# Performance work log

Measured on AMD Instinct MI355X. Metric: run time of the kernel, lower is better.

The kernel has to match this reference:

```python
import jax, jax.numpy as jnp
import numpy as np

K = 16            # neighbors
QUERY_CHUNK = 256 # SE is applied per chunk of this many query points (matches torch loop)
EPS = 1e-5        # BatchNorm eps (eval mode, running stats)


def bn(x, g, b, m, v):
    # eval-mode batchnorm over last axis (channel-last layout here)
    return (x - m) * (g / jnp.sqrt(v + EPS)) + b


def setup_inputs() -> dict:
    key = jax.random.key(0)
    ks = jax.random.split(key, 16)
    B, Cin, N = 4, 128, 4096
    H, Cout = 128, 256
    se_h = Cout // 4
    r = lambda k, s, sc=1.0: jax.random.normal(k, s, jnp.float32) * sc
    return dict(
        x=r(ks[0], (B, Cin, N)),
        W_edge=r(ks[1], (H, 2 * Cin), 0.05),          # edge_mlp conv2d 1x1
        bn1_g=jnp.ones((H,), jnp.float32), bn1_b=jnp.zeros((H,), jnp.float32),
        bn1_m=r(ks[2], (H,), 0.1), bn1_v=jax.random.uniform(ks[3], (H,), jnp.float32) + 0.5,
        w_att=r(ks[4], (H,), 0.1),                     # att_conv (1,H,1,1)
        W_fuse=r(ks[5], (Cout, H), 0.05),              # fuse conv1d
        bn2_g=jnp.ones((Cout,), jnp.float32), bn2_b=jnp.zeros((Cout,), jnp.float32),
        bn2_m=r(ks[6], (Cout,), 0.1), bn2_v=jax.random.uniform(ks[7], (Cout,), jnp.float32) + 0.5,
        fc1_w=r(ks[8], (se_h, Cout), 0.05), fc1_b=jnp.zeros((se_h,), jnp.float32),
        fc2_w=r(ks[9], (Cout, se_h), 0.05), fc2_b=jnp.zeros((Cout,), jnp.float32),
        W_res=r(ks[10], (Cout, Cin), 0.05),            # res_conv conv1d (in!=out)
        bn3_g=jnp.ones((Cout,), jnp.float32), bn3_b=jnp.zeros((Cout,), jnp.float32),
        bn3_m=r(ks[11], (Cout,), 0.1), bn3_v=jax.random.uniform(ks[12], (Cout,), jnp.float32) + 0.5,
    )


def reference(x, W_edge, bn1_g, bn1_b, bn1_m, bn1_v, w_att,
              W_fuse, bn2_g, bn2_b, bn2_m, bn2_v,
              fc1_w, fc1_b, fc2_w, fc2_b,
              W_res, bn3_g, bn3_b, bn3_m, bn3_v):
    B, Cin, N = x.shape
    x_t = jnp.swapaxes(x, 1, 2)  # (B,N,Cin)

    # KNN on features (dynamic=False -> knn on x.transpose); squared euclidean
    # has the same ordering as torch.cdist(p=2).
    sq = jnp.sum(x_t * x_t, axis=-1)                               # (B,N)
    d2 = sq[:, :, None] + sq[:, None, :] - 2.0 * jnp.einsum('bnc,bmc->bnm', x_t, x_t)
    _, idx = jax.lax.top_k(-d2, K)                                  # (B,N,K) smallest dists

    neigh = jax.vmap(lambda p, i: p[i])(x_t, idx)                   # (B,N,K,Cin)
    center = jnp.broadcast_to(x_t[:, :, None, :], neigh.shape)      # (B,N,K,Cin)
    edge = jnp.concatenate([neigh - center, center], axis=-1)       # (B,N,K,2Cin)

    # edge_mlp: 1x1 conv + BN + ReLU
    h = jax.nn.relu(bn(jnp.einsum('bnkc,hc->bnkh', edge, W_edge),
                       bn1_g, bn1_b, bn1_m, bn1_v))                 # (B,N,K,H)

    # attention over neighbors
    att = jax.nn.softmax(jnp.einsum('bnkh,h->bnk', h, w_att), axis=-1)
    agg = jnp.einsum('bnkh,bnk->bnh', h, att)                       # (B,N,H)

    # fuse conv1d + BN + ReLU
    out = jax.nn.relu(bn(jnp.einsum('bnh,oh->bno', agg, W_fuse),
                         bn2_g, bn2_b, bn2_m, bn2_v))               # (B,N,Cout)

    # SE channel attention, applied per query chunk (matches torch loop semantics)
    Cout = out.shape[-1]
    nc = N // QUERY_CHUNK
    oc = out.reshape(B, nc, QUERY_CHUNK, Cout)
    s = oc.mean(axis=2)                                             # (B,nc,Cout)
    s = jax.nn.relu(jnp.einsum('bmc,hc->bmh', s, fc1_w) + fc1_b)
    s = jax.nn.sigmoid(jnp.einsum('bmh,ch->bmc', s, fc2_w) + fc2_b)
    out = (oc * s[:, :, None, :]).reshape(B, N, Cout)

    # residual projection (in_channels != out_channels)
    res = bn(jnp.einsum('bnc,oc->bno', x_t, W_res), bn3_g, bn3_b, bn3_m, bn3_v)
    out = out + res
    return jnp.swapaxes(out, 1, 2)                                  # (B,Cout,N)
```

## Files before the change

### kernel.cpp

```cpp
#include <hip/hip_runtime.h>
#include <cstddef>

typedef __bf16 bf16;
typedef __bf16 bf16x8 __attribute__((ext_vector_type(8)));
typedef float  f32x4  __attribute__((ext_vector_type(4)));
typedef unsigned short u16;
typedef unsigned long long u64;

#define MFMA16x16(a, b, c) __builtin_amdgcn_mfma_f32_16x16x32_bf16((a), (b), (c), 0, 0, 0)

namespace {
constexpr int BB   = 4;
constexpr int CIN  = 128;
constexpr int NPT  = 4096;
constexpr int KNBR = 16;
constexpr int HED  = 128;
constexpr int COUT = 256;
}

__device__ __forceinline__ double mk_keyd(float d, unsigned mlo ) {
  const u64 k = ((u64)__float_as_uint(d) << 32) | mlo;
  return __longlong_as_double((long long)k);
}
__device__ __forceinline__ int key_idx(double kd) {
  return (int)((__double_as_longlong(kd) >> 20) & 0xFFF);
}

__device__ __forceinline__ void sort16d(double* k) {
  #pragma unroll
  for (int sz = 2; sz <= 16; sz <<= 1) {
    #pragma unroll
    for (int st = sz >> 1; st > 0; st >>= 1) {
      #pragma unroll
      for (int i = 0; i < 16; ++i) {
        const int j = i ^ st;
        if (j > i) {
          const bool up = ((i & sz) == 0);
          const double a = k[i], c = k[j];
          const double lo = fmin(a, c), hi = fmax(a, c);
          k[i] = up ? lo : hi;
          k[j] = up ? hi : lo;
        }
      }
    }
  }
}

__device__ __forceinline__ void merge16d(double* R, const double* B) {
  double t[16];
  #pragma unroll
  for (int i = 0; i < 16; ++i) t[i] = fmin(R[i], B[15 - i]);
  #pragma unroll
  for (int st = 8; st > 0; st >>= 1) {
    #pragma unroll
    for (int i = 0; i < 16; ++i) {
      const int j = i ^ st;
      if (j > i) {
        const double a = t[i], c = t[j];
        t[i] = fmin(a, c);
        t[j] = fmax(a, c);
      }
    }
  }
  #pragma unroll
  for (int i = 0; i < 16; ++i) R[i] = t[i];
}

__device__ __forceinline__ void shfl_merge16d(double* R, int mask) {
  double B[16];
  #pragma unroll
  for (int i = 0; i < 16; ++i) B[i] = __shfl_xor(R[i], mask, 64);
  merge16d(R, B);
}

__global__ __launch_bounds__(256) void k_wconv(const float* __restrict__ We,
                                               const float* __restrict__ Wf,
                                               const float* __restrict__ Wr,
                                               bf16* __restrict__ Web,
                                               bf16* __restrict__ Wfb,
                                               bf16* __restrict__ Wrb) {
  const int i = blockIdx.x * 256 + threadIdx.x;
  const int a = i >> 15;
  const int j = i & 32767;
  const float* src = (a == 0) ? We : (a == 1) ? Wf : Wr;
  bf16*        dst = (a == 0) ? Web : (a == 1) ? Wfb : Wrb;
  dst[j] = (bf16)src[j];
}

__global__ __launch_bounds__(256) void k_prep(const float* __restrict__ x,
                                              bf16* __restrict__ xh,
                                              bf16* __restrict__ xl,
                                              float* __restrict__ sq) {
  __shared__ __attribute__((aligned(16))) bf16 th[64][136];
  __shared__ __attribute__((aligned(16))) bf16 tl[64][136];
  __shared__ float sqp[4][64];
  const int tid = threadIdx.x;
  const int b   = blockIdx.x >> 6;
  const int n0  = (blockIdx.x & 63) << 6;
  const int nl  = tid & 63;
  const int cg  = tid >> 6;
  const float* xb = x + (size_t)b * CIN * NPT;
  float acc = 0.f;
  #pragma unroll
  for (int rep = 0; rep < 32; ++rep) {
    const int c = rep * 4 + cg;
    const float v = xb[(size_t)c * NPT + n0 + nl];
    const bf16 h = (bf16)v;
    const bf16 l = (bf16)(v - (float)h);
    acc += v * v;
    th[nl][c] = h;
    tl[nl][c] = l;
  }
  sqp[cg][nl] = acc;
  __syncthreads();
  bf16* xho = xh + ((size_t)b * NPT + n0) * CIN;
  bf16* xlo = xl + ((size_t)b * NPT + n0) * CIN;
  #pragma unroll
  for (int rep = 0; rep < 32; ++rep) {
    const int e = rep * 256 + tid;
    const int r = e >> 7;
    const int c = e & 127;
    xho[(size_t)r * CIN + c] = th[r][c];
    xlo[(size_t)r * CIN + c] = tl[r][c];
  }
  if (tid < 64) {
    sq[b * NPT + n0 + tid] = sqp[0][tid] + sqp[1][tid] + sqp[2][tid] + sqp[3][tid];
  }
}

__global__ __launch_bounds__(256, 2) void k_knn(const bf16* __restrict__ xh,
                                                const bf16* __restrict__ xl,
                                                const float* __restrict__ sq,
                                                int* __restrict__ knn_idx) {
  __shared__ double Lk[32][66];
  const int tid  = threadIdx.x;
  const int w    = tid >> 6;
  const int lane = tid & 63;
  const int col  = lane & 15;
  const int quad = lane >> 4;
  const int b    = blockIdx.x >> 7;
  const int q0   = (blockIdx.x & 127) << 5;
  const bf16*  xhb = xh + (size_t)b * NPT * CIN;
  const bf16*  xlb = xl + (size_t)b * NPT * CIN;
  const float* sqb = sq + b * NPT;

  bf16x8 qh[2][4], ql[2][4];
  float sqn[2];
  #pragma unroll
  for (int t = 0; t < 2; ++t) {
    const bf16* qrh = xhb + (size_t)(q0 + t * 16 + col) * CIN + quad * 8;
    const bf16* qrl = xlb + (size_t)(q0 + t * 16 + col) * CIN + quad * 8;
    #pragma unroll
    for (int ks = 0; ks < 4; ++ks) {
      qh[t][ks] = *(const bf16x8*)(qrh + ks * 32);
      ql[t][ks] = *(const bf16x8*)(qrl + ks * 32);
    }
    sqn[t] = sqb[q0 + t * 16 + col];
  }

  const double INF = __builtin_inf();
  double R0[16], R1[16];
  #pragma unroll
  for (int i = 0; i < 16; ++i) { R0[i] = INF; R1[i] = INF; }

  const int cbase = w << 10;
  for (int mt = 0; mt < 16; ++mt) {
    const int m0 = cbase + (mt << 6);
    double k0[16], k1[16];
    #pragma unroll
    for (int cb = 0; cb < 4; ++cb) {
      const bf16* crh = xhb + (size_t)(m0 + cb * 16 + col) * CIN + quad * 8;
      const bf16* crl = xlb + (size_t)(m0 + cb * 16 + col) * CIN + quad * 8;
      f32x4 a0 = {0.f, 0.f, 0.f, 0.f};
      f32x4 a1 = {0.f, 0.f, 0.f, 0.f};
      #pragma unroll
      for (int ks = 0; ks < 4; ++ks) {
        const bf16x8 ch_ = *(const bf16x8*)(crh + ks * 32);
        const bf16x8 cl_ = *(const bf16x8*)(crl + ks * 32);
        a0 = MFMA16x16(cl_, qh[0][ks], a0);
        a0 = MFMA16x16(ch_, ql[0][ks], a0);
        a0 = MFMA16x16(ch_, qh[0][ks], a0);
        a1 = MFMA16x16(cl_, qh[1][ks], a1);
        a1 = MFMA16x16(ch_, ql[1][ks], a1);
        a1 = MFMA16x16(ch_, qh[1][ks], a1);
      }
      const f32x4 sqm = *(const f32x4*)(sqb + m0 + cb * 16 + quad * 4);
      const unsigned mlo0 = (unsigned)(m0 + cb * 16 + quad * 4) << 20;
      #pragma unroll
      for (int r = 0; r < 4; ++r) {
        k0[cb * 4 + r] = mk_keyd((sqn[0] + sqm[r]) - 2.0f * a0[r], mlo0 + ((unsigned)r << 20));
        k1[cb * 4 + r] = mk_keyd((sqn[1] + sqm[r]) - 2.0f * a1[r], mlo0 + ((unsigned)r << 20));
      }
    }
    sort16d(k0); merge16d(R0, k0);
    sort16d(k1); merge16d(R1, k1);
  }

  shfl_merge16d(R0, 16);
  shfl_merge16d(R0, 32);
  shfl_merge16d(R1, 16);
  shfl_merge16d(R1, 32);

  if (quad == 0) {
    #pragma unroll
    for (int i = 0; i < 16; ++i) {
      Lk[col][w * 16 + i]        = R0[i];
      Lk[16 | col][w * 16 + i]   = R1[i];
    }
  }
  __syncthreads();

  if (tid < 64) {
    const int q = tid >> 1;
    const int j = tid & 1;
    double A[16], Bv[16];
    #pragma unroll
    for (int i = 0; i < 16; ++i) {
      A[i]  = Lk[q][(2 * j) * 16 + i];
      Bv[i] = Lk[q][(2 * j + 1) * 16 + i];
    }
    merge16d(A, Bv);
    #pragma unroll
    for (int i = 0; i < 16; ++i) Lk[q][j * 16 + i] = A[i];
  }
  __syncthreads();
  if (tid < 32) {
    double A[16], Bv[16];
    #pragma unroll
    for (int i = 0; i < 16; ++i) {
      A[i]  = Lk[tid][i];
      Bv[i] = Lk[tid][16 + i];
    }
    merge16d(A, Bv);
    int* op = knn_idx + (size_t)(b * NPT + q0 + tid) * KNBR;
    #pragma unroll
    for (int i = 0; i < 16; ++i) op[i] = key_idx(A[i]);
  }
}

__global__ __launch_bounds__(256) void k_edge(const bf16* __restrict__ xh,
                                              const bf16* __restrict__ xl,
                                              const int* __restrict__ knn_idx,
                                              const bf16* __restrict__ We,
                                              const float* __restrict__ g1, const float* __restrict__ b1,
                                              const float* __restrict__ m1, const float* __restrict__ v1,
                                              const float* __restrict__ watt,
                                              bf16* __restrict__ agg) {
  __shared__ __attribute__((aligned(16))) bf16 Ew[4][16][264];
  __shared__ float s1[HED], t1[HED], wat[HED];
  const int tid  = threadIdx.x;
  const int w    = tid >> 6;
  const int lane = tid & 63;
  const int col  = lane & 15;
  const int quad = lane >> 4;
  if (tid < HED) {
    const float ss = g1[tid] / sqrtf(v1[tid] + 1e-5f);
    s1[tid] = ss;
    t1[tid] = b1[tid] - m1[tid] * ss;
    wat[tid] = watt[tid];
  }
  __syncthreads();
  const int p = blockIdx.x * 4 + w;
  const int b = p >> 12;
  const int n = p & 4095;
  const bf16* xhb = xh + (size_t)b * NPT * CIN;
  const bf16* xlb = xl + (size_t)b * NPT * CIN;
  const int my = knn_idx[(size_t)p * KNBR + col];
  const int m  = __shfl(my, lane >> 2);
  const int sub = lane & 3;
  const int kn  = lane >> 2;
  const bf16* nh = xhb + (size_t)m * CIN + sub * 32;
  const bf16* nl_ = xlb + (size_t)m * CIN + sub * 32;
  const bf16* ch = xhb + (size_t)n * CIN + sub * 32;
  const bf16* cl = xlb + (size_t)n * CIN + sub * 32;
  #pragma unroll
  for (int j = 0; j < 4; ++j) {
    const bf16x8 nhv = *(const bf16x8*)(nh + j * 8);
    const bf16x8 nlv = *(const bf16x8*)(nl_ + j * 8);
    const bf16x8 chv = *(const bf16x8*)(ch + j * 8);
    const bf16x8 clv = *(const bf16x8*)(cl + j * 8);
    bf16x8 dv, cv;
    #pragma unroll
    for (int e = 0; e < 8; ++e) {
      const float nf = (float)nhv[e] + (float)nlv[e];
      const float cf = (float)chv[e] + (float)clv[e];
      dv[e] = (bf16)(nf - cf);
      cv[e] = (bf16)cf;
    }
    *(bf16x8*)&Ew[w][kn][sub * 32 + j * 8]       = dv;
    *(bf16x8*)&Ew[w][kn][128 + sub * 32 + j * 8] = cv;
  }
  const f32x4 zero4 = {0.f, 0.f, 0.f, 0.f};
  f32x4 acc[8];
  #pragma unroll
  for (int hb = 0; hb < 8; ++hb) acc[hb] = zero4;
  #pragma unroll
  for (int ks = 0; ks < 8; ++ks) {
    const bf16x8 af = *(const bf16x8*)&Ew[w][col][ks * 32 + quad * 8];
    #pragma unroll
    for (int hb = 0; hb < 8; ++hb) {
      const bf16x8 bfv = *(const bf16x8*)(We + (size_t)(hb * 16 + col) * 256 + ks * 32 + quad * 8);
      acc[hb] = MFMA16x16(af, bfv, acc[hb]);
    }
  }
  float h[8][4];
  float lg[4] = {0.f, 0.f, 0.f, 0.f};
  #pragma unroll
  for (int hb = 0; hb < 8; ++hb) {
    const int hc = hb * 16 + col;
    const float ss = s1[hc], tt = t1[hc], ww = wat[hc];
    #pragma unroll
    for (int r = 0; r < 4; ++r) {
      const float hv = fmaxf(acc[hb][r] * ss + tt, 0.f);
      h[hb][r] = hv;
      lg[r] += hv * ww;
    }
  }
  #pragma unroll
  for (int r = 0; r < 4; ++r) {
    float vv = lg[r];
    vv += __shfl_xor(vv, 1);
    vv += __shfl_xor(vv, 2);
    vv += __shfl_xor(vv, 4);
    vv += __shfl_xor(vv, 8);
    lg[r] = vv;
  }
  float mx = fmaxf(fmaxf(lg[0], lg[1]), fmaxf(lg[2], lg[3]));
  mx = fmaxf(mx, __shfl_xor(mx, 16));
  mx = fmaxf(mx, __shfl_xor(mx, 32));
  float ex[4];
  float sm = 0.f;
  #pragma unroll
  for (int r = 0; r < 4; ++r) { ex[r] = expf(lg[r] - mx); sm += ex[r]; }
  sm += __shfl_xor(sm, 16);
  sm += __shfl_xor(sm, 32);
  const float inv = 1.0f / sm;
  float ag[8];
  #pragma unroll
  for (int hb = 0; hb < 8; ++hb) {
    float a = h[hb][0] * ex[0] + h[hb][1] * ex[1] + h[hb][2] * ex[2] + h[hb][3] * ex[3];
    a += __shfl_xor(a, 16);
    a += __shfl_xor(a, 32);
    ag[hb] = a * inv;
  }
  if (quad == 0) {
    bf16* ao = agg + (size_t)p * HED;
    #pragma unroll
    for (int hb = 0; hb < 8; ++hb) ao[hb * 16 + col] = (bf16)ag[hb];
  }
}

__global__ __launch_bounds__(256) void k_fuse(const bf16* __restrict__ agg,
                                              const bf16* __restrict__ Wf,
                                              const float* __restrict__ g2, const float* __restrict__ b2,
                                              const float* __restrict__ m2, const float* __restrict__ v2,
                                              bf16* __restrict__ outp) {
  const int tid  = threadIdx.x;
  const int w    = tid >> 6;
  const int lane = tid & 63;
  const int col  = lane & 15;
  const int quad = lane >> 4;
  const int pb   = blockIdx.x >> 2;
  const int obq  = blockIdx.x & 3;
  const int p0   = (pb * 4 + w) * 16;
  bf16x8 afr[4];
  const bf16* arow = agg + (size_t)(p0 + col) * HED + quad * 8;
  #pragma unroll
  for (int ks = 0; ks < 4; ++ks) afr[ks] = *(const bf16x8*)(arow + ks * 32);
  #pragma unroll
  for (int i = 0; i < 4; ++i) {
    const int ob = obq * 4 + i;
    f32x4 acc = {0.f, 0.f, 0.f, 0.f};
    const bf16* brow = Wf + (size_t)(ob * 16 + col) * HED + quad * 8;
    #pragma unroll
    for (int ks = 0; ks < 4; ++ks)
      acc = MFMA16x16(afr[ks], *(const bf16x8*)(brow + ks * 32), acc);
    const int o = ob * 16 + col;
    const float ss = g2[o] / sqrtf(v2[o] + 1e-5f);
    const float tt = b2[o] - m2[o] * ss;
    #pragma unroll
    for (int r = 0; r < 4; ++r) {
      outp[(size_t)(p0 + quad * 4 + r) * COUT + o] = (bf16)fmaxf(acc[r] * ss + tt, 0.f);
    }
  }
}

__global__ __launch_bounds__(256) void k_se1(const bf16* __restrict__ outp,
                                             float* __restrict__ part) {
  const int blk = blockIdx.x;
  const int tid = threadIdx.x;
  const bf16* base = outp + ((size_t)(blk >> 2) * 256 + (size_t)(blk & 3) * 64) * COUT;
  float s = 0.f;
  for (int p2 = 0; p2 < 64; ++p2) s += (float)base[(size_t)p2 * COUT + tid];
  part[(size_t)blk * COUT + tid] = s;
}

__global__ __launch_bounds__(256) void k_se2(const float* __restrict__ part,
                                             const float* __restrict__ f1w, const float* __restrict__ f1b,
                                             const float* __restrict__ f2w, const float* __restrict__ f2b,
                                             float* __restrict__ sse) {
  __shared__ float mean_s[COUT];
  __shared__ float h1[64];
  const int bc  = blockIdx.x;
  const int tid = threadIdx.x;
  const float* pb = part + (size_t)bc * 4 * COUT;
  mean_s[tid] = (pb[tid] + pb[COUT + tid] + pb[2 * COUT + tid] + pb[3 * COUT + tid]) * (1.0f / 256.0f);
  __syncthreads();
  if (tid < 64) {
    float a = f1b[tid];
    for (int c = 0; c < COUT; ++c) a += f1w[tid * COUT + c] * mean_s[c];
    h1[tid] = fmaxf(a, 0.f);
  }
  __syncthreads();
  float a = f2b[tid];
  #pragma unroll
  for (int j = 0; j < 64; ++j) a += f2w[tid * 64 + j] * h1[j];
  sse[(size_t)bc * COUT + tid] = 1.0f / (1.0f + expf(-a));
}

__global__ __launch_bounds__(256) void k_final(const bf16* __restrict__ xh,
                                               const bf16* __restrict__ Wr,
                                               const float* __restrict__ g3, const float* __restrict__ b3,
                                               const float* __restrict__ m3, const float* __restrict__ v3,
                                               const bf16* __restrict__ outp,
                                               const float* __restrict__ sse,
                                               float* __restrict__ out) {
  const int tid  = threadIdx.x;
  const int w    = tid >> 6;
  const int lane = tid & 63;
  const int col  = lane & 15;
  const int quad = lane >> 4;
  const int pb   = blockIdx.x >> 2;
  const int obq  = blockIdx.x & 3;
  const int p0   = (pb * 4 + w) * 16;
  const int b    = p0 >> 12;
  const int n0l  = p0 & 4095;
  bf16x8 afr[4];
  const bf16* arow = xh + (size_t)(p0 + col) * CIN + quad * 8;
  #pragma unroll
  for (int ks = 0; ks < 4; ++ks) afr[ks] = *(const bf16x8*)(arow + ks * 32);
  const float* scb = sse + (size_t)(b * 16 + (n0l >> 8)) * COUT;
  #pragma unroll
  for (int i = 0; i < 4; ++i) {
    const int ob = obq * 4 + i;
    f32x4 acc = {0.f, 0.f, 0.f, 0.f};
    const bf16* brow = Wr + (size_t)(ob * 16 + col) * CIN + quad * 8;
    #pragma unroll
    for (int ks = 0; ks < 4; ++ks)
      acc = MFMA16x16(afr[ks], *(const bf16x8*)(brow + ks * 32), acc);
    const int o = ob * 16 + col;
    const float ss = g3[o] / sqrtf(v3[o] + 1e-5f);
    const float tt = b3[o] - m3[o] * ss;
    const float sc = scb[o];
    f32x4 pk;
    #pragma unroll
    for (int r = 0; r < 4; ++r) {
      const float res = acc[r] * ss + tt;
      pk[r] = (float)outp[(size_t)(p0 + quad * 4 + r) * COUT + o] * sc + res;
    }
    float* op = out + (size_t)(b * COUT + o) * NPT + n0l + quad * 4;
    *(f32x4*)op = pk;
  }
}

extern "C" void kernel_launch(void* const* d_in, const int* in_sizes, int n_in,
                              void* d_out, int out_size, void* d_ws, size_t ws_size,
                              hipStream_t stream) {
  (void)in_sizes; (void)n_in; (void)out_size; (void)ws_size;
  const float* x    = (const float*)d_in[0];
  const float* We   = (const float*)d_in[1];
  const float* g1   = (const float*)d_in[2];
  const float* b1   = (const float*)d_in[3];
  const float* m1   = (const float*)d_in[4];
  const float* v1   = (const float*)d_in[5];
  const float* watt = (const float*)d_in[6];
  const float* Wf   = (const float*)d_in[7];
  const float* g2   = (const float*)d_in[8];
  const float* b2   = (const float*)d_in[9];
  const float* m2   = (const float*)d_in[10];
  const float* v2   = (const float*)d_in[11];
  const float* f1w  = (const float*)d_in[12];
  const float* f1b  = (const float*)d_in[13];
  const float* f2w  = (const float*)d_in[14];
  const float* f2b  = (const float*)d_in[15];
  const float* Wr   = (const float*)d_in[16];
  const float* g3   = (const float*)d_in[17];
  const float* b3   = (const float*)d_in[18];
  const float* m3   = (const float*)d_in[19];
  const float* v3   = (const float*)d_in[20];

  char* ws = (char*)d_ws;
  size_t off = 0;
  bf16*  xth  = (bf16*)(ws + off);  off += (size_t)BB * NPT * CIN * 2;
  bf16*  xtl  = (bf16*)(ws + off);  off += (size_t)BB * NPT * CIN * 2;
  float* sq   = (float*)(ws + off); off += (size_t)BB * NPT * 4;
  int*   idxp = (int*)(ws + off);   off += (size_t)BB * NPT * KNBR * 4;
  bf16*  aggp = (bf16*)(ws + off);  off += (size_t)BB * NPT * HED * 2;
  bf16*  outp = (bf16*)(ws + off);  off += (size_t)BB * NPT * COUT * 2;
  float* ssep = (float*)(ws + off); off += (size_t)BB * 16 * COUT * 4;
  float* partp= (float*)(ws + off); off += (size_t)256 * COUT * 4;
  bf16*  Web  = (bf16*)(ws + off);  off += (size_t)HED * 2 * CIN * 2;
  bf16*  Wfb  = (bf16*)(ws + off);  off += (size_t)COUT * HED * 2;
  bf16*  Wrb  = (bf16*)(ws + off);  off += (size_t)COUT * CIN * 2;

  float* out = (float*)d_out;

  k_wconv<<<384, 256, 0, stream>>>(We, Wf, Wr, Web, Wfb, Wrb);
  k_prep<<<256, 256, 0, stream>>>(x, xth, xtl, sq);
  k_knn<<<512, 256, 0, stream>>>(xth, xtl, sq, idxp);
  k_edge<<<4096, 256, 0, stream>>>(xth, xtl, idxp, Web, g1, b1, m1, v1, watt, aggp);
  k_fuse<<<1024, 256, 0, stream>>>(aggp, Wfb, g2, b2, m2, v2, outp);
  k_se1<<<256, 256, 0, stream>>>(outp, partp);
  k_se2<<<64, 256, 0, stream>>>(partp, f1w, f1b, f2w, f2b, ssep);
  k_final<<<1024, 256, 0, stream>>>(xth, Wrb, g3, b3, m3, v3, outp, ssep, out);
}
```

Baseline: 421.8 us.

## Merge weight conversion into prep, fold SE sums into fuse, batch edge points

Folds the weight bf16 conversion and zeroing of the SE partial buffer into the prep kernel as extra blocks. The SE channel sums are now accumulated by the fuse kernel with shuffles plus atomics, so the separate k_se1 pass over the output is gone. The edge kernel loops over four points per wave with a quarter of the blocks, which amortises the BN/attention table setup. The aim is fewer launches and one less read of the output; the cost is atomic contention and a reduction order that is no longer deterministic.

```diff
diff --git a/kernel.cpp b/kernel.cpp
--- a/kernel.cpp
+++ b/kernel.cpp
@@ -73,30 +73,37 @@
   merge16d(R, B);
 }
 
-__global__ __launch_bounds__(256) void k_wconv(const float* __restrict__ We,
+__global__ __launch_bounds__(256) void k_prepw(const float* __restrict__ x,
+                                               bf16* __restrict__ xh,
+                                               bf16* __restrict__ xl,
+                                               float* __restrict__ sq,
+                                               const float* __restrict__ We,
                                                const float* __restrict__ Wf,
                                                const float* __restrict__ Wr,
                                                bf16* __restrict__ Web,
                                                bf16* __restrict__ Wfb,
-                                               bf16* __restrict__ Wrb) {
-  const int i = blockIdx.x * 256 + threadIdx.x;
-  const int a = i >> 15;
-  const int j = i & 32767;
-  const float* src = (a == 0) ? We : (a == 1) ? Wf : Wr;
-  bf16*        dst = (a == 0) ? Web : (a == 1) ? Wfb : Wrb;
-  dst[j] = (bf16)src[j];
-}
-
-__global__ __launch_bounds__(256) void k_prep(const float* __restrict__ x,
-                                              bf16* __restrict__ xh,
-                                              bf16* __restrict__ xl,
-                                              float* __restrict__ sq) {
+                                               bf16* __restrict__ Wrb,
+                                               float* __restrict__ partp) {
   __shared__ __attribute__((aligned(16))) bf16 th[64][136];
   __shared__ __attribute__((aligned(16))) bf16 tl[64][136];
   __shared__ float sqp[4][64];
+  const int blk = blockIdx.x;
   const int tid = threadIdx.x;
-  const int b   = blockIdx.x >> 6;
-  const int n0  = (blockIdx.x & 63) << 6;
+  if (blk >= 256) {
+    if (blk < 640) {
+      const int i = (blk - 256) * 256 + tid;
+      const int a = i >> 15;
+      const int j = i & 32767;
+      const float* src = (a == 0) ? We : (a == 1) ? Wf : Wr;
+      bf16*        dst = (a == 0) ? Web : (a == 1) ? Wfb : Wrb;
+      dst[j] = (bf16)src[j];
+    } else {
+      for (int i = tid; i < 64 * COUT; i += 256) partp[i] = 0.f;
+    }
+    return;
+  }
+  const int b   = blk >> 6;
+  const int n0  = (blk & 63) << 6;
   const int nl  = tid & 63;
   const int cg  = tid >> 6;
   const float* xb = x + (size_t)b * CIN * NPT;
@@ -260,93 +267,96 @@
     wat[tid] = watt[tid];
   }
   __syncthreads();
-  const int p = blockIdx.x * 4 + w;
-  const int b = p >> 12;
-  const int n = p & 4095;
-  const bf16* xhb = xh + (size_t)b * NPT * CIN;
-  const bf16* xlb = xl + (size_t)b * NPT * CIN;
-  const int my = knn_idx[(size_t)p * KNBR + col];
-  const int m  = __shfl(my, lane >> 2);
-  const int sub = lane & 3;
-  const int kn  = lane >> 2;
-  const bf16* nh = xhb + (size_t)m * CIN + sub * 32;
-  const bf16* nl_ = xlb + (size_t)m * CIN + sub * 32;
-  const bf16* ch = xhb + (size_t)n * CIN + sub * 32;
-  const bf16* cl = xlb + (size_t)n * CIN + sub * 32;
-  #pragma unroll
-  for (int j = 0; j < 4; ++j) {
-    const bf16x8 nhv = *(const bf16x8*)(nh + j * 8);
-    const bf16x8 nlv = *(const bf16x8*)(nl_ + j * 8);
-    const bf16x8 chv = *(const bf16x8*)(ch + j * 8);
-    const bf16x8 clv = *(const bf16x8*)(cl + j * 8);
-    bf16x8 dv, cv;
-    #pragma unroll
-    for (int e = 0; e < 8; ++e) {
-      const float nf = (float)nhv[e] + (float)nlv[e];
-      const float cf = (float)chv[e] + (float)clv[e];
-      dv[e] = (bf16)(nf - cf);
-      cv[e] = (bf16)cf;
-    }
-    *(bf16x8*)&Ew[w][kn][sub * 32 + j * 8]       = dv;
-    *(bf16x8*)&Ew[w][kn][128 + sub * 32 + j * 8] = cv;
-  }
-  const f32x4 zero4 = {0.f, 0.f, 0.f, 0.f};
-  f32x4 acc[8];
-  #pragma unroll
-  for (int hb = 0; hb < 8; ++hb) acc[hb] = zero4;
-  #pragma unroll
-  for (int ks = 0; ks < 8; ++ks) {
-    const bf16x8 af = *(const bf16x8*)&Ew[w][col][ks * 32 + quad * 8];
+  const int gw = blockIdx.x * 4 + w;
+  for (int it = 0; it < 4; ++it) {
+    const int p = gw * 4 + it;
+    const int b = p >> 12;
+    const int n = p & 4095;
+    const bf16* xhb = xh + (size_t)b * NPT * CIN;
+    const bf16* xlb = xl + (size_t)b * NPT * CIN;
+    const int my = knn_idx[(size_t)p * KNBR + col];
+    const int m  = __shfl(my, lane >> 2);
+    const int sub = lane & 3;
+    const int kn  = lane >> 2;
+    const bf16* nh = xhb + (size_t)m * CIN + sub * 32;
+    const bf16* nl_ = xlb + (size_t)m * CIN + sub * 32;
+    const bf16* ch = xhb + (size_t)n * CIN + sub * 32;
+    const bf16* cl = xlb + (size_t)n * CIN + sub * 32;
+    #pragma unroll
+    for (int j = 0; j < 4; ++j) {
+      const bf16x8 nhv = *(const bf16x8*)(nh + j * 8);
+      const bf16x8 nlv = *(const bf16x8*)(nl_ + j * 8);
+      const bf16x8 chv = *(const bf16x8*)(ch + j * 8);
+      const bf16x8 clv = *(const bf16x8*)(cl + j * 8);
+      bf16x8 dv, cv;
+      #pragma unroll
+      for (int e = 0; e < 8; ++e) {
+        const float nf = (float)nhv[e] + (float)nlv[e];
+        const float cf = (float)chv[e] + (float)clv[e];
+        dv[e] = (bf16)(nf - cf);
+        cv[e] = (bf16)cf;
+      }
+      *(bf16x8*)&Ew[w][kn][sub * 32 + j * 8]       = dv;
+      *(bf16x8*)&Ew[w][kn][128 + sub * 32 + j * 8] = cv;
+    }
+    const f32x4 zero4 = {0.f, 0.f, 0.f, 0.f};
+    f32x4 acc[8];
+    #pragma unroll
+    for (int hb = 0; hb < 8; ++hb) acc[hb] = zero4;
+    #pragma unroll
+    for (int ks = 0; ks < 8; ++ks) {
+      const bf16x8 af = *(const bf16x8*)&Ew[w][col][ks * 32 + quad * 8];
+      #pragma unroll
+      for (int hb = 0; hb < 8; ++hb) {
+        const bf16x8 bfv = *(const bf16x8*)(We + (size_t)(hb * 16 + col) * 256 + ks * 32 + quad * 8);
+        acc[hb] = MFMA16x16(af, bfv, acc[hb]);
+      }
+    }
+    float h[8][4];
+    float lg[4] = {0.f, 0.f, 0.f, 0.f};
     #pragma unroll
     for (int hb = 0; hb < 8; ++hb) {
-      const bf16x8 bfv = *(const bf16x8*)(We + (size_t)(hb * 16 + col) * 256 + ks * 32 + quad * 8);
-      acc[hb] = MFMA16x16(af, bfv, acc[hb]);
-    }
-  }
-  float h[8][4];
-  float lg[4] = {0.f, 0.f, 0.f, 0.f};
-  #pragma unroll
-  for (int hb = 0; hb < 8; ++hb) {
-    const int hc = hb * 16 + col;
-    const float ss = s1[hc], tt = t1[hc], ww = wat[hc];
+      const int hc = hb * 16 + col;
+      const float ss = s1[hc], tt = t1[hc], ww = wat[hc];
+      #pragma unroll
+      for (int r = 0; r < 4; ++r) {
+        const float hv = fmaxf(acc[hb][r] * ss + tt, 0.f);
+        h[hb][r] = hv;
+        lg[r] += hv * ww;
+      }
+    }
     #pragma unroll
     for (int r = 0; r < 4; ++r) {
-      const float hv = fmaxf(acc[hb][r] * ss + tt, 0.f);
-      h[hb][r] = hv;
-      lg[r] += hv * ww;
-    }
-  }
-  #pragma unroll
-  for (int r = 0; r < 4; ++r) {
-    float vv = lg[r];
-    vv += __shfl_xor(vv, 1);
-    vv += __shfl_xor(vv, 2);
-    vv += __shfl_xor(vv, 4);
-    vv += __shfl_xor(vv, 8);
-    lg[r] = vv;
-  }
-  float mx = fmaxf(fmaxf(lg[0], lg[1]), fmaxf(lg[2], lg[3]));
-  mx = fmaxf(mx, __shfl_xor(mx, 16));
-  mx = fmaxf(mx, __shfl_xor(mx, 32));
-  float ex[4];
-  float sm = 0.f;
-  #pragma unroll
-  for (int r = 0; r < 4; ++r) { ex[r] = expf(lg[r] - mx); sm += ex[r]; }
-  sm += __shfl_xor(sm, 16);
-  sm += __shfl_xor(sm, 32);
-  const float inv = 1.0f / sm;
-  float ag[8];
-  #pragma unroll
-  for (int hb = 0; hb < 8; ++hb) {
-    float a = h[hb][0] * ex[0] + h[hb][1] * ex[1] + h[hb][2] * ex[2] + h[hb][3] * ex[3];
-    a += __shfl_xor(a, 16);
-    a += __shfl_xor(a, 32);
-    ag[hb] = a * inv;
-  }
-  if (quad == 0) {
-    bf16* ao = agg + (size_t)p * HED;
-    #pragma unroll
-    for (int hb = 0; hb < 8; ++hb) ao[hb * 16 + col] = (bf16)ag[hb];
+      float vv = lg[r];
+      vv += __shfl_xor(vv, 1);
+      vv += __shfl_xor(vv, 2);
+      vv += __shfl_xor(vv, 4);
+      vv += __shfl_xor(vv, 8);
+      lg[r] = vv;
+    }
+    float mx = fmaxf(fmaxf(lg[0], lg[1]), fmaxf(lg[2], lg[3]));
+    mx = fmaxf(mx, __shfl_xor(mx, 16));
+    mx = fmaxf(mx, __shfl_xor(mx, 32));
+    float ex[4];
+    float sm = 0.f;
+    #pragma unroll
+    for (int r = 0; r < 4; ++r) { ex[r] = expf(lg[r] - mx); sm += ex[r]; }
+    sm += __shfl_xor(sm, 16);
+    sm += __shfl_xor(sm, 32);
+    const float inv = 1.0f / sm;
+    float ag[8];
+    #pragma unroll
+    for (int hb = 0; hb < 8; ++hb) {
+      float a = h[hb][0] * ex[0] + h[hb][1] * ex[1] + h[hb][2] * ex[2] + h[hb][3] * ex[3];
+      a += __shfl_xor(a, 16);
+      a += __shfl_xor(a, 32);
+      ag[hb] = a * inv;
+    }
+    if (quad == 0) {
+      bf16* ao = agg + (size_t)p * HED;
+      #pragma unroll
+      for (int hb = 0; hb < 8; ++hb) ao[hb * 16 + col] = (bf16)ag[hb];
+    }
   }
 }
 
@@ -354,7 +364,8 @@
                                               const bf16* __restrict__ Wf,
                                               const float* __restrict__ g2, const float* __restrict__ b2,
                                               const float* __restrict__ m2, const float* __restrict__ v2,
-                                              bf16* __restrict__ outp) {
+                                              bf16* __restrict__ outp,
+                                              float* __restrict__ partp) {
   const int tid  = threadIdx.x;
   const int w    = tid >> 6;
   const int lane = tid & 63;
@@ -363,6 +374,7 @@
   const int pb   = blockIdx.x >> 2;
   const int obq  = blockIdx.x & 3;
   const int p0   = (pb * 4 + w) * 16;
+  const int bc   = p0 >> 8;
   bf16x8 afr[4];
   const bf16* arow = agg + (size_t)(p0 + col) * HED + quad * 8;
   #pragma unroll
@@ -378,24 +390,20 @@
     const int o = ob * 16 + col;
     const float ss = g2[o] / sqrtf(v2[o] + 1e-5f);
     const float tt = b2[o] - m2[o] * ss;
+    float se_s = 0.f;
     #pragma unroll
     for (int r = 0; r < 4; ++r) {
-      outp[(size_t)(p0 + quad * 4 + r) * COUT + o] = (bf16)fmaxf(acc[r] * ss + tt, 0.f);
-    }
-  }
-}
-
-__global__ __launch_bounds__(256) void k_se1(const bf16* __restrict__ outp,
-                                             float* __restrict__ part) {
-  const int blk = blockIdx.x;
-  const int tid = threadIdx.x;
-  const bf16* base = outp + ((size_t)(blk >> 2) * 256 + (size_t)(blk & 3) * 64) * COUT;
-  float s = 0.f;
-  for (int p2 = 0; p2 < 64; ++p2) s += (float)base[(size_t)p2 * COUT + tid];
-  part[(size_t)blk * COUT + tid] = s;
-}
-
-__global__ __launch_bounds__(256) void k_se2(const float* __restrict__ part,
+      const float v = fmaxf(acc[r] * ss + tt, 0.f);
+      outp[(size_t)(p0 + quad * 4 + r) * COUT + o] = (bf16)v;
+      se_s += v;
+    }
+    se_s += __shfl_xor(se_s, 16);
+    se_s += __shfl_xor(se_s, 32);
+    if (quad == 0) atomicAdd(&partp[(size_t)bc * COUT + o], se_s);
+  }
+}
+
+__global__ __launch_bounds__(256) void k_se2(const float* __restrict__ partp,
                                              const float* __restrict__ f1w, const float* __restrict__ f1b,
                                              const float* __restrict__ f2w, const float* __restrict__ f2b,
                                              float* __restrict__ sse) {
@@ -403,8 +411,7 @@
   __shared__ float h1[64];
   const int bc  = blockIdx.x;
   const int tid = threadIdx.x;
-  const float* pb = part + (size_t)bc * 4 * COUT;
-  mean_s[tid] = (pb[tid] + pb[COUT + tid] + pb[2 * COUT + tid] + pb[3 * COUT + tid]) * (1.0f / 256.0f);
+  mean_s[tid] = partp[(size_t)bc * COUT + tid] * (1.0f / 256.0f);
   __syncthreads();
   if (tid < 64) {
     float a = f1b[tid];
@@ -498,19 +505,17 @@
   bf16*  aggp = (bf16*)(ws + off);  off += (size_t)BB * NPT * HED * 2;
   bf16*  outp = (bf16*)(ws + off);  off += (size_t)BB * NPT * COUT * 2;
   float* ssep = (float*)(ws + off); off += (size_t)BB * 16 * COUT * 4;
-  float* partp= (float*)(ws + off); off += (size_t)256 * COUT * 4;
+  float* partp= (float*)(ws + off); off += (size_t)64 * COUT * 4;
   bf16*  Web  = (bf16*)(ws + off);  off += (size_t)HED * 2 * CIN * 2;
   bf16*  Wfb  = (bf16*)(ws + off);  off += (size_t)COUT * HED * 2;
   bf16*  Wrb  = (bf16*)(ws + off);  off += (size_t)COUT * CIN * 2;
 
   float* out = (float*)d_out;
 
-  k_wconv<<<384, 256, 0, stream>>>(We, Wf, Wr, Web, Wfb, Wrb);
-  k_prep<<<256, 256, 0, stream>>>(x, xth, xtl, sq);
+  k_prepw<<<641, 256, 0, stream>>>(x, xth, xtl, sq, We, Wf, Wr, Web, Wfb, Wrb, partp);
   k_knn<<<512, 256, 0, stream>>>(xth, xtl, sq, idxp);
-  k_edge<<<4096, 256, 0, stream>>>(xth, xtl, idxp, Web, g1, b1, m1, v1, watt, aggp);
-  k_fuse<<<1024, 256, 0, stream>>>(aggp, Wfb, g2, b2, m2, v2, outp);
-  k_se1<<<256, 256, 0, stream>>>(outp, partp);
+  k_edge<<<1024, 256, 0, stream>>>(xth, xtl, idxp, Web, g1, b1, m1, v1, watt, aggp);
+  k_fuse<<<1024, 256, 0, stream>>>(aggp, Wfb, g2, b2, m2, v2, outp, partp);
   k_se2<<<64, 256, 0, stream>>>(partp, f1w, f1b, f2w, f2b, ssep);
   k_final<<<1024, 256, 0, stream>>>(xth, Wrb, g3, b3, m3, v3, outp, ssep, out);
 }
```

After: 369.2 us. 1.14x faster.
